# Kernel optimization log

Hardware: AMD Instinct MI355X
Metric: run time of the kernel (lower is better)

## Reference

```python
import jax, jax.numpy as jnp
import numpy as np
from jax import tree_util

H = 64; V = 64; INNER = 32; STEPS = 3
LR = 0.05; B1 = 0.9; B2 = 0.999; EPS = 1e-8
B = 256; L = 2048


def setup_inputs() -> dict:
    key = jax.random.key(0)
    ks = jax.random.split(key, 8)
    def rn(k, shape, s):
        return jax.random.normal(k, shape, jnp.float32) * s
    return dict(
        seq=jax.random.randint(ks[0], (B, L), 0, V),
        emb=rn(ks[1], (V, H), 0.02),
        ff_w1=rn(ks[2], (2 * H, H), (1.0 / H) ** 0.5), ff_b1=jnp.zeros((2 * H,), jnp.float32),
        ff_w2=rn(ks[3], (H, 2 * H), (1.0 / (2 * H)) ** 0.5), ff_b2=jnp.zeros((H,), jnp.float32),
        ln_g=jnp.ones((H,), jnp.float32), ln_b=jnp.zeros((H,), jnp.float32),
        fc1_w=rn(ks[4], (INNER, H), (1.0 / H) ** 0.5), fc1_b=jnp.zeros((INNER,), jnp.float32),
        fc2_w=rn(ks[5], (H, INNER), (1.0 / INNER) ** 0.5), fc2_b=jnp.zeros((H,), jnp.float32),
        out_w=rn(ks[6], (V, H), (1.0 / H) ** 0.5), out_b=jnp.zeros((V,), jnp.float32),
    )


def _inner_loss(params, k, v):
    w1, b1, w2, b2 = params
    pred = jnp.maximum(k @ w1.T + b1, 0.0) @ w2.T + b2
    return jnp.mean((pred - v) ** 2)


def reference(seq, emb, ff_w1, ff_b1, ff_w2, ff_b2, ln_g, ln_b,
              fc1_w, fc1_b, fc2_w, fc2_b, out_w, out_b):
    # Encoder: embed -> FFN residual -> LayerNorm
    e = emb[seq]                                             # [B, L, H]
    ff = jnp.maximum(e @ ff_w1.T + ff_b1, 0.0) @ ff_w2.T + ff_b2
    x = e + ff
    mu = x.mean(-1, keepdims=True)
    var = ((x - mu) ** 2).mean(-1, keepdims=True)
    hs = (x - mu) / jnp.sqrt(var + 1e-5) * ln_g + ln_b       # [B, L, H]

    # Torch detaches hs / params inside the inner loop, so no grad flows there.
    hs_d = jax.lax.stop_gradient(hs)
    ts = np.arange(0, L - 3, 2)                              # T = 1023 steps per pass
    kh = jnp.tile(hs_d[:, ts], (1, STEPS, 1))                # [B, STEPS*T, H]
    vh = jnp.tile(hs_d[:, ts + 1], (1, STEPS, 1))
    qh = hs_d[:, -1]                                         # [B, H]
    p0 = tuple(jax.lax.stop_gradient(p) for p in (fc1_w, fc1_b, fc2_w, fc2_b))

    def run_one(khs, vhs, q):
        zeros = tuple(jnp.zeros_like(p) for p in p0)

        def step(carry, kv):
            params, m1, m2, n = carry
            k, v = kv
            g = jax.grad(_inner_loss)(params, k, v)
            n1 = n + 1.0
            c1 = 1.0 - B1 ** n1
            c2 = 1.0 - B2 ** n1
            m1n = tree_util.tree_map(lambda m, gg: B1 * m + (1 - B1) * gg, m1, g)
            m2n = tree_util.tree_map(lambda m, gg: B2 * m + (1 - B2) * gg * gg, m2, g)
            pn = tree_util.tree_map(
                lambda p, a, b: p - LR * (a / c1) / (jnp.sqrt(b / c2) + EPS),
                params, m1n, m2n)
            return (pn, m1n, m2n, n1), None

        (pf, _, _, _), _ = jax.lax.scan(step, (p0, zeros, zeros, jnp.float32(0.0)), (khs, vhs))
        w1, b1, w2, b2 = pf
        return jnp.maximum(q @ w1.T + b1, 0.0) @ w2.T + b2

    ctxs = jax.vmap(run_one)(kh, vh, qh)                     # [B, H]
    return ctxs @ out_w.T + out_b                            # [B, V]
```

## Files before the change

### kernel.cpp

```cpp
#include <hip/hip_runtime.h>


typedef float v2f __attribute__((ext_vector_type(2)));

__device__ __forceinline__ v2f mk2(float a, float b) { v2f r; r.x = a; r.y = b; return r; }

__device__ __forceinline__ v2f pk_fma(v2f a, v2f b, v2f c) {
  return __builtin_elementwise_fma(a, b, c);
}
__device__ __forceinline__ v2f pk_mul(v2f a, v2f b) { return a * b; }

template <int CTRL>
__device__ __forceinline__ float dpp_add(float x) {
  union { float f; int i; } u, r;
  u.f = x;
  r.i = __builtin_amdgcn_update_dpp(0, u.i, CTRL, 0xF, 0xF, true);
  return x + r.f;
}

__device__ __forceinline__ void adam_upd(float& p, float& m1, float& m2,
                                         float g, float c2inv, float nls)
{
  m1 = fmaf(0.9f,  m1, 0.1f   * g);
  m2 = fmaf(0.999f, m2, 0.001f * (g * g));
  float den = __builtin_amdgcn_sqrtf(m2 * c2inv) + 1e-8f;
  p = fmaf(nls * m1, __builtin_amdgcn_rcpf(den), p);
}

__device__ __forceinline__ void adam_upd2(v2f& p, v2f& m1, v2f& m2,
                                          v2f g, v2f c2inv2, v2f nls2)
{
  m1 = pk_fma(mk2(0.9f, 0.9f),   m1, pk_mul(mk2(0.1f, 0.1f),   g));
  m2 = pk_fma(mk2(0.999f, 0.999f), m2,
              pk_mul(mk2(0.001f, 0.001f), pk_mul(g, g)));
  v2f d2 = pk_mul(m2, c2inv2);
  v2f den = mk2(__builtin_amdgcn_sqrtf(d2.x) + 1e-8f,
                __builtin_amdgcn_sqrtf(d2.y) + 1e-8f);
  v2f rec = mk2(__builtin_amdgcn_rcpf(den.x), __builtin_amdgcn_rcpf(den.y));
  p = pk_fma(pk_mul(nls2, m1), rec, p);
}

__global__ void prep_kernel(const float* __restrict__ emb,
                            const float* __restrict__ ffw1, const float* __restrict__ ffb1,
                            const float* __restrict__ ffw2, const float* __restrict__ ffb2,
                            const float* __restrict__ lng,  const float* __restrict__ lnb,
                            float* __restrict__ hs_out)
{
  const int v = blockIdx.x;
  const int t = threadIdx.x;
  __shared__ float e[64];
  __shared__ float r[128];
  if (t < 64) e[t] = emb[v * 64 + t];
  __syncthreads();
  {
    float s = ffb1[t];
    const float* wrow = ffw1 + t * 64;
#pragma unroll 8
    for (int m = 0; m < 64; ++m) s = fmaf(wrow[m], e[m], s);
    r[t] = fmaxf(s, 0.f);
  }
  __syncthreads();
  if (t < 64) {
    float s = ffb2[t];
    const float* wrow = ffw2 + t * 128;
#pragma unroll 8
    for (int o = 0; o < 128; ++o) s = fmaf(wrow[o], r[o], s);
    float x = e[t] + s;
    float mu = x;
    for (int m = 1; m < 64; m <<= 1) mu += __shfl_xor(mu, m, 64);
    mu *= (1.f / 64.f);
    float dv = x - mu;
    float var = dv * dv;
    for (int m = 1; m < 64; m <<= 1) var += __shfl_xor(var, m, 64);
    var *= (1.f / 64.f);
    float hs = dv / sqrtf(var + 1e-5f);
    hs_out[v * 64 + t] = hs * lng[t] + lnb[t];
  }
}

__global__ __launch_bounds__(64)
void table_kernel(float* __restrict__ tab)
{
  if (threadIdx.x != 0) return;
  double pb1 = 1.0, pb2 = 1.0;
  for (int n = 0; n < 3069; ++n) {
    pb1 *= 0.9; pb2 *= 0.999;
    float c1inv = __builtin_amdgcn_rcpf((float)(1.0 - pb1));
    float c2inv = __builtin_amdgcn_rcpf((float)(1.0 - pb2));
    tab[2 * n]     = -0.05f * c1inv;
    tab[2 * n + 1] = c2inv;
  }
}

__global__ __launch_bounds__(512)
void scan_kernel(const int* __restrict__ seq, const float* __restrict__ hs_tab,
                 const float* __restrict__ tab_g,
                 const float* __restrict__ fc1w, const float* __restrict__ fc1b,
                 const float* __restrict__ fc2w, const float* __restrict__ fc2b,
                 const float* __restrict__ outw, const float* __restrict__ outb,
                 float* __restrict__ out)
{
  const int b      = blockIdx.x;
  const int t      = threadIdx.x;
  const bool isw2  = (t < 256);
  const int tl     = t & 255;
  const int lane   = tl & 63;
  const int wv     = tl >> 6;
  const int i1     = tl >> 3;
  const int j0     = (tl & 7) << 3;
  const int p0     = i1 << 1;
  const int c0     = (tl & 7) << 2;
  const int sub    = tl & 7;

  __shared__ __align__(16) float hs[4096];
  __shared__ __align__(16) int   sq[2048];
  __shared__ __align__(16) float tabs[6144];
  __shared__ __align__(16) float h_s[32];
  __shared__ __align__(16) float dhp[32][20];
  __shared__ __align__(16) float ctx[64];

  for (int i = t; i < 1024; i += 512)
    ((float4*)hs)[i] = ((const float4*)hs_tab)[i];
  {
    const int4* sg = (const int4*)(seq + (long long)b * 2048);
    ((int4*)sq)[t] = sg[t];
  }
  for (int i = t; i < 1536; i += 512)
    ((float4*)tabs)[i] = ((const float4*)tab_g)[i];

  v2f w1p[4], m1a2[4], m2a2[4];
  float b1v = 0.f, m1c = 0.f, m2c = 0.f;
  v2f w2p[4], m1b2[4], m2b2[4];
  v2f b2v2 = mk2(0.f, 0.f), m1d2 = mk2(0.f, 0.f), m2d2 = mk2(0.f, 0.f);
#pragma unroll
  for (int j = 0; j < 4; ++j) {
    w1p[j] = mk2(0.f, 0.f); m1a2[j] = mk2(0.f, 0.f); m2a2[j] = mk2(0.f, 0.f);
    w2p[j] = mk2(0.f, 0.f); m1b2[j] = mk2(0.f, 0.f); m2b2[j] = mk2(0.f, 0.f);
  }
  if (isw2) {
    w2p[0] = mk2(fc2w[p0 * 32 + c0 + 0], fc2w[p0 * 32 + c0 + 1]);
    w2p[1] = mk2(fc2w[p0 * 32 + c0 + 2], fc2w[p0 * 32 + c0 + 3]);
    w2p[2] = mk2(fc2w[(p0 + 1) * 32 + c0 + 0], fc2w[(p0 + 1) * 32 + c0 + 1]);
    w2p[3] = mk2(fc2w[(p0 + 1) * 32 + c0 + 2], fc2w[(p0 + 1) * 32 + c0 + 3]);
    b2v2 = mk2(fc2b[p0], fc2b[p0 + 1]);
  } else {
#pragma unroll
    for (int j = 0; j < 4; ++j)
      w1p[j] = mk2(fc1w[i1 * 64 + j0 + 2 * j], fc1w[i1 * 64 + j0 + 2 * j + 1]);
    b1v = fc1b[i1];
  }

  __syncthreads();

  const int qtok = sq[2047];

  int2 p1 = *(const int2*)(sq + 2);
  int ka1 = p1.x, vb1 = p1.y;
  int jn = 2;

  float kk[8], hv = 0.f;
  float v0 = 0.f, v1 = 0.f;

  if (!isw2) {
    const int ka = sq[0];
    const float4 k0 = *(const float4*)(hs + ka * 64 + j0);
    const float4 k1 = *(const float4*)(hs + ka * 64 + j0 + 4);
    kk[0]=k0.x; kk[1]=k0.y; kk[2]=k0.z; kk[3]=k0.w;
    kk[4]=k1.x; kk[5]=k1.y; kk[6]=k1.z; kk[7]=k1.w;
    float pa = 0.f;
    pa = fmaf(w1p[0].x, kk[0], pa);
    pa = fmaf(w1p[0].y, kk[1], pa);
    pa = fmaf(w1p[1].x, kk[2], pa);
    pa = fmaf(w1p[1].y, kk[3], pa);
    pa = fmaf(w1p[2].x, kk[4], pa);
    pa = fmaf(w1p[2].y, kk[5], pa);
    pa = fmaf(w1p[3].x, kk[6], pa);
    pa = fmaf(w1p[3].y, kk[7], pa);
    pa = dpp_add<0xB1>(pa);
    pa = dpp_add<0x4E>(pa);
    pa = dpp_add<0x141>(pa);
    hv = fmaxf(pa + b1v, 0.f);
    if (sub == 1) h_s[i1] = hv;
  } else {
    const int vb = sq[1];
    v0 = hs[vb * 64 + p0];
    v1 = hs[vb * 64 + p0 + 1];
  }
  __syncthreads();

  for (int step = 0; step < 3069; ++step) {
    const v2f tc = *(const v2f*)(tabs + 2 * step);
    const float nls = tc.x, c2inv = tc.y;
    const v2f nls2 = mk2(nls, nls), c2inv2 = mk2(c2inv, c2inv);

    float kn[8];
    v2f hh0 = mk2(0.f, 0.f), hh1 = mk2(0.f, 0.f);
    float dd0 = 0.f, dd1 = 0.f;

    const int2 rd = *(const int2*)(sq + 2 * jn);
    const int kaN = (step <= 3066) ? rd.x : qtok;
    const int vbN = (step <= 3066) ? rd.y : 0;
    jn = (jn == 1022) ? 0 : jn + 1;

    if (isw2) {
      const float4 h4 = *(const float4*)(h_s + c0);
      hh0 = mk2(h4.x, h4.y); hh1 = mk2(h4.z, h4.w);
      float q0 = 0.f, q1 = 0.f;
      q0 = fmaf(w2p[0].x, hh0.x, q0);  q1 = fmaf(w2p[2].x, hh0.x, q1);
      q0 = fmaf(w2p[0].y, hh0.y, q0);  q1 = fmaf(w2p[2].y, hh0.y, q1);
      q0 = fmaf(w2p[1].x, hh1.x, q0);  q1 = fmaf(w2p[3].x, hh1.x, q1);
      q0 = fmaf(w2p[1].y, hh1.y, q0);  q1 = fmaf(w2p[3].y, hh1.y, q1);
      q0 = dpp_add<0xB1>(q0);   q1 = dpp_add<0xB1>(q1);
      q0 = dpp_add<0x4E>(q0);   q1 = dpp_add<0x4E>(q1);
      q0 = dpp_add<0x141>(q0);  q1 = dpp_add<0x141>(q1);
      dd0 = 0.03125f * (q0 + b2v2.x - v0);
      dd1 = 0.03125f * (q1 + b2v2.y - v1);

      float dp[4];
      dp[0] = fmaf(w2p[2].x, dd1, w2p[0].x * dd0);
      dp[1] = fmaf(w2p[2].y, dd1, w2p[0].y * dd0);
      dp[2] = fmaf(w2p[3].x, dd1, w2p[1].x * dd0);
      dp[3] = fmaf(w2p[3].y, dd1, w2p[1].y * dd0);
#pragma unroll
      for (int ii = 0; ii < 4; ++ii) dp[ii] = dpp_add<0x128>(dp[ii]);
      if (!(lane & 8)) {
        const int slot = wv * 4 + (lane >> 4);
        const int colb = (lane & 7) << 2;
        dhp[colb + 0][slot] = dp[0];
        dhp[colb + 1][slot] = dp[1];
        dhp[colb + 2][slot] = dp[2];
        dhp[colb + 3][slot] = dp[3];
      }
    } else {
      const float4 k0 = *(const float4*)(hs + ka1 * 64 + j0);
      const float4 k1 = *(const float4*)(hs + ka1 * 64 + j0 + 4);
      kn[0]=k0.x; kn[1]=k0.y; kn[2]=k0.z; kn[3]=k0.w;
      kn[4]=k1.x; kn[5]=k1.y; kn[6]=k1.z; kn[7]=k1.w;
    }
    __syncthreads();

    if (isw2) {
      const float vn0 = hs[vb1 * 64 + p0];
      const float vn1 = hs[vb1 * 64 + p0 + 1];
      adam_upd2(w2p[0], m1b2[0], m2b2[0], pk_mul(mk2(dd0, dd0), hh0), c2inv2, nls2);
      adam_upd2(w2p[1], m1b2[1], m2b2[1], pk_mul(mk2(dd0, dd0), hh1), c2inv2, nls2);
      adam_upd2(w2p[2], m1b2[2], m2b2[2], pk_mul(mk2(dd1, dd1), hh0), c2inv2, nls2);
      adam_upd2(w2p[3], m1b2[3], m2b2[3], pk_mul(mk2(dd1, dd1), hh1), c2inv2, nls2);
      adam_upd2(b2v2, m1d2, m2d2, mk2(dd0, dd1), c2inv2, nls2);
      v0 = vn0; v1 = vn1;
    } else {
      const float4 pA = *(const float4*)&dhp[i1][0];
      const float4 pB = *(const float4*)&dhp[i1][4];
      const float4 pC = *(const float4*)&dhp[i1][8];
      const float4 pD = *(const float4*)&dhp[i1][12];
      const float W0 = (pA.x + pA.y) + (pA.z + pA.w);
      const float W1 = (pB.x + pB.y) + (pB.z + pB.w);
      const float W2 = (pC.x + pC.y) + (pC.z + pC.w);
      const float W3 = (pD.x + pD.y) + (pD.z + pD.w);
      const float dhsum = (W0 + W1) + (W2 + W3);
      const float dh = (hv > 0.f) ? dhsum : 0.f;
      const v2f dh2 = mk2(dh, dh);
      adam_upd2(w1p[0], m1a2[0], m2a2[0],
                pk_mul(dh2, mk2(kk[0], kk[1])), c2inv2, nls2);
      adam_upd2(w1p[1], m1a2[1], m2a2[1],
                pk_mul(dh2, mk2(kk[2], kk[3])), c2inv2, nls2);
      adam_upd2(w1p[2], m1a2[2], m2a2[2],
                pk_mul(dh2, mk2(kk[4], kk[5])), c2inv2, nls2);
      adam_upd2(w1p[3], m1a2[3], m2a2[3],
                pk_mul(dh2, mk2(kk[6], kk[7])), c2inv2, nls2);
      adam_upd(b1v, m1c, m2c, dh, c2inv, nls);
#pragma unroll
      for (int jj = 0; jj < 8; ++jj) kk[jj] = kn[jj];
      float pa = 0.f;
      pa = fmaf(w1p[0].x, kk[0], pa);
      pa = fmaf(w1p[0].y, kk[1], pa);
      pa = fmaf(w1p[1].x, kk[2], pa);
      pa = fmaf(w1p[1].y, kk[3], pa);
      pa = fmaf(w1p[2].x, kk[4], pa);
      pa = fmaf(w1p[2].y, kk[5], pa);
      pa = fmaf(w1p[3].x, kk[6], pa);
      pa = fmaf(w1p[3].y, kk[7], pa);
      pa = dpp_add<0xB1>(pa);
      pa = dpp_add<0x4E>(pa);
      pa = dpp_add<0x141>(pa);
      hv = fmaxf(pa + b1v, 0.f);
      if (sub == 1) h_s[i1] = hv;
    }
    ka1 = kaN; vb1 = vbN;
    __syncthreads();
  }

  if (isw2) {
    const float4 h4 = *(const float4*)(h_s + c0);
    float q0 = 0.f, q1 = 0.f;
    q0 = fmaf(w2p[0].x, h4.x, q0); q1 = fmaf(w2p[2].x, h4.x, q1);
    q0 = fmaf(w2p[0].y, h4.y, q0); q1 = fmaf(w2p[2].y, h4.y, q1);
    q0 = fmaf(w2p[1].x, h4.z, q0); q1 = fmaf(w2p[3].x, h4.z, q1);
    q0 = fmaf(w2p[1].y, h4.w, q0); q1 = fmaf(w2p[3].y, h4.w, q1);
    q0 = dpp_add<0xB1>(q0);   q1 = dpp_add<0xB1>(q1);
    q0 = dpp_add<0x4E>(q0);   q1 = dpp_add<0x4E>(q1);
    q0 = dpp_add<0x141>(q0);  q1 = dpp_add<0x141>(q1);
    if (sub == 2) { ctx[p0] = q0 + b2v2.x; ctx[p0 + 1] = q1 + b2v2.y; }
  }
  __syncthreads();

  if (t < 64) {
    float acc = outb[t];
    const float* wrow = outw + t * 64;
#pragma unroll 8
    for (int p = 0; p < 64; ++p) acc = fmaf(wrow[p], ctx[p], acc);
    out[(long long)b * 64 + t] = acc;
  }
}

extern "C" void kernel_launch(void* const* d_in, const int* in_sizes, int n_in,
                              void* d_out, int out_size, void* d_ws, size_t ws_size,
                              hipStream_t stream) {
  const int*   seq  = (const int*)  d_in[0];
  const float* emb  = (const float*)d_in[1];
  const float* ffw1 = (const float*)d_in[2];
  const float* ffb1 = (const float*)d_in[3];
  const float* ffw2 = (const float*)d_in[4];
  const float* ffb2 = (const float*)d_in[5];
  const float* lng  = (const float*)d_in[6];
  const float* lnb  = (const float*)d_in[7];
  const float* fc1w = (const float*)d_in[8];
  const float* fc1b = (const float*)d_in[9];
  const float* fc2w = (const float*)d_in[10];
  const float* fc2b = (const float*)d_in[11];
  const float* outw = (const float*)d_in[12];
  const float* outb = (const float*)d_in[13];
  float* out    = (float*)d_out;
  float* hs_tab = (float*)d_ws;
  float* tab    = (float*)d_ws + 4096;

  prep_kernel<<<64, 128, 0, stream>>>(emb, ffw1, ffb1, ffw2, ffb2, lng, lnb, hs_tab);
  table_kernel<<<1, 64, 0, stream>>>(tab);
  scan_kernel<<<256, 512, 0, stream>>>(seq, hs_tab, tab, fc1w, fc1b, fc2w, fc2b,
                                       outw, outb, out);
}
```

Baseline: 2.626 ms.

## Pack four batch rows per block and merge the w1/w2 thread roles

Each 1024-thread block now runs four independent batch scans, and every thread handles both the fc2 and fc1 parts of a step instead of splitting them across two thread halves. The Adam schedule table is no longer staged into LDS; it is prefetched one step ahead from global memory. The value rows are prefetched alongside the key rows, and the fc2 Adam update moves ahead of the first barrier. The intent is to shorten per-step barrier handoffs and LDS traffic. In exchange the grid drops to 64 blocks, leaving most CUs idle and putting more serial work on each wave.

```diff
diff --git a/kernel.cpp b/kernel.cpp
--- a/kernel.cpp
+++ b/kernel.cpp
@@ -92,7 +92,7 @@
   }
 }
 
-__global__ __launch_bounds__(512)
+__global__ __launch_bounds__(1024)
 void scan_kernel(const int* __restrict__ seq, const float* __restrict__ hs_tab,
                  const float* __restrict__ tab_g,
                  const float* __restrict__ fc1w, const float* __restrict__ fc1b,
@@ -100,73 +100,64 @@
                  const float* __restrict__ outw, const float* __restrict__ outb,
                  float* __restrict__ out)
 {
-  const int b      = blockIdx.x;
-  const int t      = threadIdx.x;
-  const bool isw2  = (t < 256);
-  const int tl     = t & 255;
-  const int lane   = tl & 63;
-  const int wv     = tl >> 6;
-  const int i1     = tl >> 3;
-  const int j0     = (tl & 7) << 3;
-  const int p0     = i1 << 1;
-  const int c0     = (tl & 7) << 2;
-  const int sub    = tl & 7;
+  const int tid  = threadIdx.x;
+  const int sc   = tid >> 8;
+  const int t    = tid & 255;
+  const int b    = blockIdx.x * 4 + sc;
+  const int lane = t & 63;
+  const int wv   = t >> 6;
+  const int i1   = t >> 3;
+  const int j0   = (t & 7) << 3;
+  const int p0   = i1 << 1;
+  const int c0   = (t & 7) << 2;
+  const int sub  = t & 7;
 
   __shared__ __align__(16) float hs[4096];
-  __shared__ __align__(16) int   sq[2048];
-  __shared__ __align__(16) float tabs[6144];
-  __shared__ __align__(16) float h_s[32];
-  __shared__ __align__(16) float dhp[32][20];
-  __shared__ __align__(16) float ctx[64];
-
-  for (int i = t; i < 1024; i += 512)
-    ((float4*)hs)[i] = ((const float4*)hs_tab)[i];
+  __shared__ __align__(16) int   sq[4][2048];
+  __shared__ __align__(16) float h_s[4][32];
+  __shared__ __align__(16) float dhp[4][32][20];
+  __shared__ __align__(16) float ctx[4][64];
+
+  ((float4*)hs)[tid] = ((const float4*)hs_tab)[tid];
   {
     const int4* sg = (const int4*)(seq + (long long)b * 2048);
-    ((int4*)sq)[t] = sg[t];
-  }
-  for (int i = t; i < 1536; i += 512)
-    ((float4*)tabs)[i] = ((const float4*)tab_g)[i];
+    ((int4*)sq[sc])[t]       = sg[t];
+    ((int4*)sq[sc])[t + 256] = sg[t + 256];
+  }
 
   v2f w1p[4], m1a2[4], m2a2[4];
-  float b1v = 0.f, m1c = 0.f, m2c = 0.f;
+  float b1v, m1c = 0.f, m2c = 0.f;
   v2f w2p[4], m1b2[4], m2b2[4];
-  v2f b2v2 = mk2(0.f, 0.f), m1d2 = mk2(0.f, 0.f), m2d2 = mk2(0.f, 0.f);
+  v2f b2v2, m1d2 = mk2(0.f, 0.f), m2d2 = mk2(0.f, 0.f);
 #pragma unroll
   for (int j = 0; j < 4; ++j) {
-    w1p[j] = mk2(0.f, 0.f); m1a2[j] = mk2(0.f, 0.f); m2a2[j] = mk2(0.f, 0.f);
-    w2p[j] = mk2(0.f, 0.f); m1b2[j] = mk2(0.f, 0.f); m2b2[j] = mk2(0.f, 0.f);
-  }
-  if (isw2) {
-    w2p[0] = mk2(fc2w[p0 * 32 + c0 + 0], fc2w[p0 * 32 + c0 + 1]);
-    w2p[1] = mk2(fc2w[p0 * 32 + c0 + 2], fc2w[p0 * 32 + c0 + 3]);
-    w2p[2] = mk2(fc2w[(p0 + 1) * 32 + c0 + 0], fc2w[(p0 + 1) * 32 + c0 + 1]);
-    w2p[3] = mk2(fc2w[(p0 + 1) * 32 + c0 + 2], fc2w[(p0 + 1) * 32 + c0 + 3]);
-    b2v2 = mk2(fc2b[p0], fc2b[p0 + 1]);
-  } else {
+    m1a2[j] = mk2(0.f, 0.f); m2a2[j] = mk2(0.f, 0.f);
+    m1b2[j] = mk2(0.f, 0.f); m2b2[j] = mk2(0.f, 0.f);
+  }
+  w2p[0] = mk2(fc2w[p0 * 32 + c0 + 0], fc2w[p0 * 32 + c0 + 1]);
+  w2p[1] = mk2(fc2w[p0 * 32 + c0 + 2], fc2w[p0 * 32 + c0 + 3]);
+  w2p[2] = mk2(fc2w[(p0 + 1) * 32 + c0 + 0], fc2w[(p0 + 1) * 32 + c0 + 1]);
+  w2p[3] = mk2(fc2w[(p0 + 1) * 32 + c0 + 2], fc2w[(p0 + 1) * 32 + c0 + 3]);
+  b2v2 = mk2(fc2b[p0], fc2b[p0 + 1]);
 #pragma unroll
-    for (int j = 0; j < 4; ++j)
-      w1p[j] = mk2(fc1w[i1 * 64 + j0 + 2 * j], fc1w[i1 * 64 + j0 + 2 * j + 1]);
-    b1v = fc1b[i1];
-  }
-
-  __syncthreads();
-
-  const int qtok = sq[2047];
-
-  int2 p1 = *(const int2*)(sq + 2);
-  int ka1 = p1.x, vb1 = p1.y;
-  int jn = 2;
-
-  float kk[8], hv = 0.f;
-  float v0 = 0.f, v1 = 0.f;
-
-  if (!isw2) {
-    const int ka = sq[0];
+  for (int j = 0; j < 4; ++j)
+    w1p[j] = mk2(fc1w[i1 * 64 + j0 + 2 * j], fc1w[i1 * 64 + j0 + 2 * j + 1]);
+  b1v = fc1b[i1];
+
+  __syncthreads();
+
+  float nls_c = tab_g[0], c2i_c = tab_g[1];
+  int jm = 1;
+  float kk[8], hv, v0, v1;
+
+  {
+    const int ka = sq[sc][0], vb = sq[sc][1];
     const float4 k0 = *(const float4*)(hs + ka * 64 + j0);
     const float4 k1 = *(const float4*)(hs + ka * 64 + j0 + 4);
     kk[0]=k0.x; kk[1]=k0.y; kk[2]=k0.z; kk[3]=k0.w;
     kk[4]=k1.x; kk[5]=k1.y; kk[6]=k1.z; kk[7]=k1.w;
+    v0 = hs[vb * 64 + p0];
+    v1 = hs[vb * 64 + p0 + 1];
     float pa = 0.f;
     pa = fmaf(w1p[0].x, kk[0], pa);
     pa = fmaf(w1p[0].y, kk[1], pa);
@@ -180,42 +171,50 @@
     pa = dpp_add<0x4E>(pa);
     pa = dpp_add<0x141>(pa);
     hv = fmaxf(pa + b1v, 0.f);
-    if (sub == 1) h_s[i1] = hv;
-  } else {
-    const int vb = sq[1];
-    v0 = hs[vb * 64 + p0];
-    v1 = hs[vb * 64 + p0 + 1];
+    if (sub == 1) h_s[sc][i1] = hv;
   }
   __syncthreads();
 
   for (int step = 0; step < 3069; ++step) {
-    const v2f tc = *(const v2f*)(tabs + 2 * step);
-    const float nls = tc.x, c2inv = tc.y;
+    const float nls = nls_c, c2inv = c2i_c;
+    {
+      const int ni = (step < 3068) ? (step + 1) : 3068;
+      nls_c = tab_g[2 * ni];
+      c2i_c = tab_g[2 * ni + 1];
+    }
     const v2f nls2 = mk2(nls, nls), c2inv2 = mk2(c2inv, c2inv);
 
-    float kn[8];
-    v2f hh0 = mk2(0.f, 0.f), hh1 = mk2(0.f, 0.f);
-    float dd0 = 0.f, dd1 = 0.f;
-
-    const int2 rd = *(const int2*)(sq + 2 * jn);
-    const int kaN = (step <= 3066) ? rd.x : qtok;
-    const int vbN = (step <= 3066) ? rd.y : 0;
-    jn = (jn == 1022) ? 0 : jn + 1;
-
-    if (isw2) {
-      const float4 h4 = *(const float4*)(h_s + c0);
-      hh0 = mk2(h4.x, h4.y); hh1 = mk2(h4.z, h4.w);
-      float q0 = 0.f, q1 = 0.f;
-      q0 = fmaf(w2p[0].x, hh0.x, q0);  q1 = fmaf(w2p[2].x, hh0.x, q1);
-      q0 = fmaf(w2p[0].y, hh0.y, q0);  q1 = fmaf(w2p[2].y, hh0.y, q1);
-      q0 = fmaf(w2p[1].x, hh1.x, q0);  q1 = fmaf(w2p[3].x, hh1.x, q1);
-      q0 = fmaf(w2p[1].y, hh1.y, q0);  q1 = fmaf(w2p[3].y, hh1.y, q1);
-      q0 = dpp_add<0xB1>(q0);   q1 = dpp_add<0xB1>(q1);
-      q0 = dpp_add<0x4E>(q0);   q1 = dpp_add<0x4E>(q1);
-      q0 = dpp_add<0x141>(q0);  q1 = dpp_add<0x141>(q1);
-      dd0 = 0.03125f * (q0 + b2v2.x - v0);
-      dd1 = 0.03125f * (q1 + b2v2.y - v1);
-
+    float kn[8], v0n, v1n;
+    {
+      int ka, vb;
+      if (step < 3068) {
+        ka = sq[sc][2 * jm]; vb = sq[sc][2 * jm + 1];
+        jm = (jm == 1022) ? 0 : jm + 1;
+      } else {
+        ka = sq[sc][2047]; vb = 0;
+      }
+      const float4 k0 = *(const float4*)(hs + ka * 64 + j0);
+      const float4 k1 = *(const float4*)(hs + ka * 64 + j0 + 4);
+      kn[0]=k0.x; kn[1]=k0.y; kn[2]=k0.z; kn[3]=k0.w;
+      kn[4]=k1.x; kn[5]=k1.y; kn[6]=k1.z; kn[7]=k1.w;
+      v0n = hs[vb * 64 + p0];
+      v1n = hs[vb * 64 + p0 + 1];
+    }
+
+    const float4 h4 = *(const float4*)(&h_s[sc][c0]);
+    const v2f hh0 = mk2(h4.x, h4.y), hh1 = mk2(h4.z, h4.w);
+    float q0 = 0.f, q1 = 0.f;
+    q0 = fmaf(w2p[0].x, hh0.x, q0);  q1 = fmaf(w2p[2].x, hh0.x, q1);
+    q0 = fmaf(w2p[0].y, hh0.y, q0);  q1 = fmaf(w2p[2].y, hh0.y, q1);
+    q0 = fmaf(w2p[1].x, hh1.x, q0);  q1 = fmaf(w2p[3].x, hh1.x, q1);
+    q0 = fmaf(w2p[1].y, hh1.y, q0);  q1 = fmaf(w2p[3].y, hh1.y, q1);
+    q0 = dpp_add<0xB1>(q0);   q1 = dpp_add<0xB1>(q1);
+    q0 = dpp_add<0x4E>(q0);   q1 = dpp_add<0x4E>(q1);
+    q0 = dpp_add<0x141>(q0);  q1 = dpp_add<0x141>(q1);
+    const float dd0 = 0.03125f * (q0 + b2v2.x - v0);
+    const float dd1 = 0.03125f * (q1 + b2v2.y - v1);
+
+    {
       float dp[4];
       dp[0] = fmaf(w2p[2].x, dd1, w2p[0].x * dd0);
       dp[1] = fmaf(w2p[2].y, dd1, w2p[0].y * dd0);
@@ -226,33 +225,25 @@
       if (!(lane & 8)) {
         const int slot = wv * 4 + (lane >> 4);
         const int colb = (lane & 7) << 2;
-        dhp[colb + 0][slot] = dp[0];
-        dhp[colb + 1][slot] = dp[1];
-        dhp[colb + 2][slot] = dp[2];
-        dhp[colb + 3][slot] = dp[3];
+        dhp[sc][colb + 0][slot] = dp[0];
+        dhp[sc][colb + 1][slot] = dp[1];
+        dhp[sc][colb + 2][slot] = dp[2];
+        dhp[sc][colb + 3][slot] = dp[3];
       }
-    } else {
-      const float4 k0 = *(const float4*)(hs + ka1 * 64 + j0);
-      const float4 k1 = *(const float4*)(hs + ka1 * 64 + j0 + 4);
-      kn[0]=k0.x; kn[1]=k0.y; kn[2]=k0.z; kn[3]=k0.w;
-      kn[4]=k1.x; kn[5]=k1.y; kn[6]=k1.z; kn[7]=k1.w;
-    }
+    }
+
+    adam_upd2(w2p[0], m1b2[0], m2b2[0], pk_mul(mk2(dd0, dd0), hh0), c2inv2, nls2);
+    adam_upd2(w2p[1], m1b2[1], m2b2[1], pk_mul(mk2(dd0, dd0), hh1), c2inv2, nls2);
+    adam_upd2(w2p[2], m1b2[2], m2b2[2], pk_mul(mk2(dd1, dd1), hh0), c2inv2, nls2);
+    adam_upd2(w2p[3], m1b2[3], m2b2[3], pk_mul(mk2(dd1, dd1), hh1), c2inv2, nls2);
+    adam_upd2(b2v2, m1d2, m2d2, mk2(dd0, dd1), c2inv2, nls2);
     __syncthreads();
 
-    if (isw2) {
-      const float vn0 = hs[vb1 * 64 + p0];
-      const float vn1 = hs[vb1 * 64 + p0 + 1];
-      adam_upd2(w2p[0], m1b2[0], m2b2[0], pk_mul(mk2(dd0, dd0), hh0), c2inv2, nls2);
-      adam_upd2(w2p[1], m1b2[1], m2b2[1], pk_mul(mk2(dd0, dd0), hh1), c2inv2, nls2);
-      adam_upd2(w2p[2], m1b2[2], m2b2[2], pk_mul(mk2(dd1, dd1), hh0), c2inv2, nls2);
-      adam_upd2(w2p[3], m1b2[3], m2b2[3], pk_mul(mk2(dd1, dd1), hh1), c2inv2, nls2);
-      adam_upd2(b2v2, m1d2, m2d2, mk2(dd0, dd1), c2inv2, nls2);
-      v0 = vn0; v1 = vn1;
-    } else {
-      const float4 pA = *(const float4*)&dhp[i1][0];
-      const float4 pB = *(const float4*)&dhp[i1][4];
-      const float4 pC = *(const float4*)&dhp[i1][8];
-      const float4 pD = *(const float4*)&dhp[i1][12];
+    {
+      const float4 pA = *(const float4*)&dhp[sc][i1][0];
+      const float4 pB = *(const float4*)&dhp[sc][i1][4];
+      const float4 pC = *(const float4*)&dhp[sc][i1][8];
+      const float4 pD = *(const float4*)&dhp[sc][i1][12];
       const float W0 = (pA.x + pA.y) + (pA.z + pA.w);
       const float W1 = (pB.x + pB.y) + (pB.z + pB.w);
       const float W2 = (pC.x + pC.y) + (pC.z + pC.w);
@@ -269,8 +260,12 @@
       adam_upd2(w1p[3], m1a2[3], m2a2[3],
                 pk_mul(dh2, mk2(kk[6], kk[7])), c2inv2, nls2);
       adam_upd(b1v, m1c, m2c, dh, c2inv, nls);
+    }
+
+    {
 #pragma unroll
       for (int jj = 0; jj < 8; ++jj) kk[jj] = kn[jj];
+      v0 = v0n; v1 = v1n;
       float pa = 0.f;
       pa = fmaf(w1p[0].x, kk[0], pa);
       pa = fmaf(w1p[0].y, kk[1], pa);
@@ -284,14 +279,13 @@
       pa = dpp_add<0x4E>(pa);
       pa = dpp_add<0x141>(pa);
       hv = fmaxf(pa + b1v, 0.f);
-      if (sub == 1) h_s[i1] = hv;
-    }
-    ka1 = kaN; vb1 = vbN;
+      if (sub == 1) h_s[sc][i1] = hv;
+    }
     __syncthreads();
   }
 
-  if (isw2) {
-    const float4 h4 = *(const float4*)(h_s + c0);
+  {
+    const float4 h4 = *(const float4*)(&h_s[sc][c0]);
     float q0 = 0.f, q1 = 0.f;
     q0 = fmaf(w2p[0].x, h4.x, q0); q1 = fmaf(w2p[2].x, h4.x, q1);
     q0 = fmaf(w2p[0].y, h4.y, q0); q1 = fmaf(w2p[2].y, h4.y, q1);
@@ -300,7 +294,7 @@
     q0 = dpp_add<0xB1>(q0);   q1 = dpp_add<0xB1>(q1);
     q0 = dpp_add<0x4E>(q0);   q1 = dpp_add<0x4E>(q1);
     q0 = dpp_add<0x141>(q0);  q1 = dpp_add<0x141>(q1);
-    if (sub == 2) { ctx[p0] = q0 + b2v2.x; ctx[p0 + 1] = q1 + b2v2.y; }
+    if (sub == 2) { ctx[sc][p0] = q0 + b2v2.x; ctx[sc][p0 + 1] = q1 + b2v2.y; }
   }
   __syncthreads();
 
@@ -308,7 +302,7 @@
     float acc = outb[t];
     const float* wrow = outw + t * 64;
 #pragma unroll 8
-    for (int p = 0; p < 64; ++p) acc = fmaf(wrow[p], ctx[p], acc);
+    for (int p = 0; p < 64; ++p) acc = fmaf(wrow[p], ctx[sc][p], acc);
     out[(long long)b * 64 + t] = acc;
   }
 }
@@ -336,6 +330,6 @@
 
   prep_kernel<<<64, 128, 0, stream>>>(emb, ffw1, ffb1, ffw2, ffb2, lng, lnb, hs_tab);
   table_kernel<<<1, 64, 0, stream>>>(tab);
-  scan_kernel<<<256, 512, 0, stream>>>(seq, hs_tab, tab, fc1w, fc1b, fc2w, fc2b,
+  scan_kernel<<<64, 1024, 0, stream>>>(seq, hs_tab, tab, fc1w, fc1b, fc2w, fc2b,
                                        outw, outb, out);
 }
```

New measurement: 6.282 ms. 2.39x slower.
